# Kernel optimization log

Measured on AMD Instinct MI355X. Metric: run time of the kernel, lower is better.

Reference implementation:

```python
import jax, jax.numpy as jnp
import numpy as np

L = 16      # number of prior layers backsubstituted through (layer_idx)
D = 1024    # uniform layer width


def setup_inputs() -> dict:
    key = jax.random.key(0)
    ks = jax.random.split(key, 8)
    weights = jax.random.normal(ks[0], (D, D), jnp.float32) / np.sqrt(D)
    biases = jax.random.normal(ks[1], (D, 1), jnp.float32)
    net_x_lowers = jax.random.normal(ks[2], (L, D, D), jnp.float32) / np.sqrt(D)
    net_x_uppers = jax.random.normal(ks[3], (L, D, D), jnp.float32) / np.sqrt(D)
    net_b_lowers = jax.random.normal(ks[4], (L, D, 1), jnp.float32)
    net_b_uppers = jax.random.normal(ks[5], (L, D, 1), jnp.float32)
    input_lowers = jax.random.normal(ks[6], (D, 1), jnp.float32)
    input_uppers = input_lowers + jax.random.uniform(ks[7], (D, 1), jnp.float32)
    return {
        "weights": weights,
        "biases": biases,
        "net_x_lowers": net_x_lowers,
        "net_x_uppers": net_x_uppers,
        "net_b_lowers": net_b_lowers,
        "net_b_uppers": net_b_uppers,
        "input_lowers": input_lowers,
        "input_uppers": input_uppers,
    }


def _backsubstitute(weights, biases, net_x_lowers, net_x_uppers,
                    net_b_lowers, net_b_uppers, input_lowers, input_uppers):
    # Initial relational bounds of the affine layer: y = W^T x + b exactly.
    x0 = weights.T  # (out, in)

    def step(carry, layer):
        xl, xu, bl, bu = carry
        A_lo, A_up, c_lo, c_up = layer
        pl = jnp.maximum(xl, 0.0)
        nl = jnp.minimum(xl, 0.0)
        pu = jnp.maximum(xu, 0.0)
        nu = jnp.minimum(xu, 0.0)
        # intercept accumulation (signed split)
        bl = bl + pl @ c_lo + nl @ c_up
        bu = bu + pu @ c_up + nu @ c_lo
        # coefficient backsubstitution (signed split)
        xl = pl @ A_lo + nl @ A_up
        xu = pu @ A_up + nu @ A_lo
        return (xl, xu, bl, bu), None

    # Loop order: network[layer_idx - i] for i = 0..L-1; the stacked arrays are
    # ordered so index i corresponds to layer (layer_idx - i).
    (xl, xu, bl, bu), _ = jax.lax.scan(
        step,
        (x0, x0, biases, biases),
        (net_x_lowers, net_x_uppers, net_b_lowers, net_b_uppers),
    )

    lo_T = input_lowers.T  # (1, d0)
    up_T = input_uppers.T
    lowers = jnp.sum(jnp.maximum(xl, 0.0) * lo_T + jnp.minimum(xl, 0.0) * up_T,
                     axis=1, keepdims=True) + bl
    uppers = jnp.sum(jnp.maximum(xu, 0.0) * up_T + jnp.minimum(xu, 0.0) * lo_T,
                     axis=1, keepdims=True) + bu
    return jnp.stack([lowers, uppers])  # (2, D, 1)


def reference(weights, biases, net_x_lowers, net_x_uppers,
              net_b_lowers, net_b_uppers, input_lowers, input_uppers):
    return _backsubstitute(weights, biases, net_x_lowers, net_x_uppers,
                           net_b_lowers, net_b_uppers, input_lowers, input_uppers)
```

## Files before the change

### kernel.cpp

```cpp
#include <hip/hip_runtime.h>


#define DD 1024
#define LL 16

typedef _Float16 f16x8 __attribute__((ext_vector_type(8)));
typedef _Float16 f16x4 __attribute__((ext_vector_type(4)));
typedef float f32x4 __attribute__((ext_vector_type(4)));

__device__ __forceinline__ void gload16(const void* gsrc, void* ldst) {
  __builtin_amdgcn_global_load_lds(
      (const __attribute__((address_space(1))) unsigned int*)gsrc,
      (__attribute__((address_space(3))) unsigned int*)ldst, 16, 0, 0);
}

struct GemmTabs {
  const _Float16* xs[2][6];
  const _Float16* as[2][6];
};

template<int NSPLIT>
__global__ __launch_bounds__(256)
void gemm_step(GemmTabs tabs, float* __restrict__ part)
{
  constexpr int KSPL = 6144 / NSPLIT;
  constexpr int NIT  = KSPL / 32;
  constexpr int NZ   = 2 * NSPLIT;

  __shared__ _Float16 smX[2][8][512];
  __shared__ _Float16 smA[2][8][512];

  const int tid  = threadIdx.x;
  const int w    = tid >> 6;
  const int lane = tid & 63;
  const int ln15 = lane & 15;
  const int lhi  = lane >> 4;

  const int lin = blockIdx.x + gridDim.x * (blockIdx.y + gridDim.y * blockIdx.z);
  const int zz  = lin % NZ;
  const int ij  = lin / NZ;
  const int j0  = (ij & 7) * 128;
  const int i0  = (ij >> 3) * 128;
  const int lu    = zz >> (NSPLIT == 6 ? 0 : 0) ? 0 : 0;
  const int lu_   = zz / NSPLIT;
  const int split = zz % NSPLIT;

  const _Float16* const* xtab = tabs.xs[lu_];
  const _Float16* const* atab = tabs.as[lu_];

  const int wm = w >> 1, wn = w & 1;

  const int kbase = split * KSPL;
  const int seg0  = kbase >> 10;
  const int segB_ = (seg0 + 1 < 6) ? seg0 + 1 : 5;
  const int it_sw = (((seg0 + 1) << 10) - kbase) >> 5;
  const _Float16* xpA = xtab[seg0];
  const _Float16* apA = atab[seg0];
  const _Float16* xpB = xtab[segB_];
  const _Float16* apB = atab[segB_];

  f32x4 acc[4][4];
#pragma unroll
  for (int a = 0; a < 4; ++a)
#pragma unroll
    for (int b = 0; b < 4; ++b) acc[a][b] = (f32x4){0.f, 0.f, 0.f, 0.f};

  const int b_it = (4096 - kbase) >> 5;

  auto stage = [&](int buf, int it) {
    const _Float16* xp = (it < it_sw) ? xpA : xpB;
    const _Float16* ap = (it < it_sw) ? apA : apB;
    const int kcol = ((kbase + it * 32) & 1023) + lhi * 8;
#pragma unroll
    for (int r = 0; r < 4; ++r) {
      const int f = r * 4 + w;
      if (f < 8)
        gload16(xp + (size_t)(i0 + f * 16 + ln15) * DD + kcol, &smX[buf][f & 7][0]);
      else
        gload16(ap + (size_t)(j0 + (f - 8) * 16 + ln15) * DD + kcol, &smA[buf][f & 7][0]);
    }
  };

  stage(0, 0);

  int buf = 0;
  for (int it = 0; it < NIT; ++it) {
    if (it + 1 < NIT) {
      stage(buf ^ 1, it + 1);
      asm volatile("s_waitcnt vmcnt(4)" ::: "memory");
    } else {
      asm volatile("s_waitcnt vmcnt(0)" ::: "memory");
    }
    __builtin_amdgcn_s_barrier();
    __builtin_amdgcn_sched_barrier(0);

    if (it == b_it) {
#pragma unroll
      for (int a = 0; a < 4; ++a)
#pragma unroll
        for (int b = 0; b < 4; ++b) acc[a][b] *= (1.f / 2048.f);
    }

    f16x8 xf[4], af[4];
#pragma unroll
    for (int mi = 0; mi < 4; ++mi)
      xf[mi] = *(const f16x8*)&smX[buf][wm * 4 + mi][lane * 8];
#pragma unroll
    for (int ni = 0; ni < 4; ++ni)
      af[ni] = *(const f16x8*)&smA[buf][wn * 4 + ni][lane * 8];
#pragma unroll
    for (int mi = 0; mi < 4; ++mi)
#pragma unroll
      for (int ni = 0; ni < 4; ++ni)
        acc[mi][ni] = __builtin_amdgcn_mfma_f32_16x16x32_f16(xf[mi], af[ni], acc[mi][ni], 0, 0, 0);

    __builtin_amdgcn_sched_barrier(0);
    if (it + 1 < NIT) __builtin_amdgcn_s_barrier();
    buf ^= 1;
  }

  const float eps = (b_it >= NIT) ? (1.f / 2048.f) : 1.f;
  float* outp = part + ((size_t)(split * 2 + lu_) << 20);
#pragma unroll
  for (int mi = 0; mi < 4; ++mi) {
    const int r0 = i0 + wm * 64 + mi * 16 + lhi * 4;
#pragma unroll
    for (int ni = 0; ni < 4; ++ni) {
      const int c = j0 + wn * 64 + ni * 16 + ln15;
#pragma unroll
      for (int e = 0; e < 4; ++e)
        outp[(size_t)(r0 + e) * DD + c] = acc[mi][ni][e] * eps;
    }
  }
}

template<int NS>
__global__ __launch_bounds__(256)
void convert_prep(int direct,
                  const float* __restrict__ xt, const float* __restrict__ part,
                  const float* __restrict__ cl, const float* __restrict__ cu,
                  _Float16* __restrict__ pl1, _Float16* __restrict__ pl2,
                  _Float16* __restrict__ nl1, _Float16* __restrict__ nl2,
                  _Float16* __restrict__ pu1, _Float16* __restrict__ pu2,
                  _Float16* __restrict__ nu1, _Float16* __restrict__ nu2,
                  float* __restrict__ bl, float* __restrict__ bu,
                  const float* __restrict__ AloN, const float* __restrict__ AupN,
                  _Float16* __restrict__ L1, _Float16* __restrict__ L2,
                  _Float16* __restrict__ U1, _Float16* __restrict__ U2)
{
  __shared__ float shmem[64][68];
  const int t = threadIdx.x;

  if (blockIdx.x < 1024) {
    const int i = blockIdx.x;
    const int k = t * 4;
    const size_t off = (size_t)i * DD + k;

    float Yl[4], Yu[4];
    if (direct) {
      const float4 y = *(const float4*)&xt[off];
      Yl[0] = Yu[0] = y.x; Yl[1] = Yu[1] = y.y; Yl[2] = Yu[2] = y.z; Yl[3] = Yu[3] = y.w;
    } else {
#pragma unroll
      for (int e = 0; e < 4; ++e) { Yl[e] = 0.f; Yu[e] = 0.f; }
#pragma unroll
      for (int s = 0; s < NS; ++s) {
        const float4 a = *(const float4*)&part[((size_t)(s * 2 + 0) << 20) + off];
        const float4 b = *(const float4*)&part[((size_t)(s * 2 + 1) << 20) + off];
        Yl[0] += a.x; Yl[1] += a.y; Yl[2] += a.z; Yl[3] += a.w;
        Yu[0] += b.x; Yu[1] += b.y; Yu[2] += b.z; Yu[3] += b.w;
      }
    }

    const float4 c4l = *(const float4*)&cl[k];
    const float4 c4u = *(const float4*)&cu[k];
    const float Cl[4] = {c4l.x, c4l.y, c4l.z, c4l.w};
    const float Cu[4] = {c4u.x, c4u.y, c4u.z, c4u.w};

    f16x4 o_pl1, o_pl2, o_nl1, o_nl2, o_pu1, o_pu2, o_nu1, o_nu2;
    float blp = 0.f, bup = 0.f;
#pragma unroll
    for (int e = 0; e < 4; ++e) {
      const float pl = fmaxf(Yl[e], 0.f), nl = fminf(Yl[e], 0.f);
      const float pu = fmaxf(Yu[e], 0.f), nu = fminf(Yu[e], 0.f);
      blp += pl * Cl[e] + nl * Cu[e];
      bup += pu * Cu[e] + nu * Cl[e];
      _Float16 h;
      h = (_Float16)pl; o_pl1[e] = h; o_pl2[e] = (_Float16)((pl - (float)h) * 2048.f);
      h = (_Float16)nl; o_nl1[e] = h; o_nl2[e] = (_Float16)((nl - (float)h) * 2048.f);
      h = (_Float16)pu; o_pu1[e] = h; o_pu2[e] = (_Float16)((pu - (float)h) * 2048.f);
      h = (_Float16)nu; o_nu1[e] = h; o_nu2[e] = (_Float16)((nu - (float)h) * 2048.f);
    }
    *(f16x4*)&pl1[off] = o_pl1;  *(f16x4*)&pl2[off] = o_pl2;
    *(f16x4*)&nl1[off] = o_nl1;  *(f16x4*)&nl2[off] = o_nl2;
    *(f16x4*)&pu1[off] = o_pu1;  *(f16x4*)&pu2[off] = o_pu2;
    *(f16x4*)&nu1[off] = o_nu1;  *(f16x4*)&nu2[off] = o_nu2;

#pragma unroll
    for (int o = 32; o > 0; o >>= 1) {
      blp += __shfl_down(blp, o, 64);
      bup += __shfl_down(bup, o, 64);
    }
    if ((t & 63) == 0) { shmem[0][t >> 6] = blp; shmem[1][t >> 6] = bup; }
    __syncthreads();
    if (t == 0) {
      bl[i] += shmem[0][0] + shmem[0][1] + shmem[0][2] + shmem[0][3];
      bu[i] += shmem[1][0] + shmem[1][1] + shmem[1][2] + shmem[1][3];
    }
  } else {
    const int r = blockIdx.x - 1024;
    const int k0 = (r & 15) * 64;
    const int n0 = ((r >> 4) & 15) * 64;
    const int zz = r >> 8;
    const int rid = t >> 4, cid = t & 15;
    const float* src = zz ? AupN : AloN;
    _Float16* d1 = zz ? U1 : L1;
    _Float16* d2 = zz ? U2 : L2;
#pragma unroll
    for (int rr = 0; rr < 4; ++rr) {
      const int kk = rid * 4 + rr;
      *(float4*)&shmem[kk][cid * 4] = *(const float4*)&src[(size_t)(k0 + kk) * DD + n0 + cid * 4];
    }
    __syncthreads();
#pragma unroll
    for (int rr = 0; rr < 4; ++rr) {
      const int n = rid * 4 + rr;
      f16x4 v1, v2;
#pragma unroll
      for (int e = 0; e < 4; ++e) {
        const float v = shmem[cid * 4 + e][n];
        const _Float16 h = (_Float16)v;
        v1[e] = h;
        v2[e] = (_Float16)((v - (float)h) * 2048.f);
      }
      const size_t o = (size_t)(n0 + n) * DD + k0 + cid * 4;
      *(f16x4*)&d1[o] = v1;
      *(f16x4*)&d2[o] = v2;
    }
  }
}

__global__ __launch_bounds__(256)
void transpose_w(const float* __restrict__ W, float* __restrict__ xt)
{
  __shared__ float tile[32][33];
  const int x  = blockIdx.x * 32 + threadIdx.x;
  const int y0 = blockIdx.y * 32 + threadIdx.y;
#pragma unroll
  for (int r = 0; r < 32; r += 8)
    tile[threadIdx.y + r][threadIdx.x] = W[(size_t)(y0 + r) * DD + x];
  __syncthreads();
  const int xo  = blockIdx.y * 32 + threadIdx.x;
  const int yo0 = blockIdx.x * 32 + threadIdx.y;
#pragma unroll
  for (int r = 0; r < 32; r += 8)
    xt[(size_t)(yo0 + r) * DD + xo] = tile[threadIdx.x][threadIdx.y + r];
}

template<int NS>
__global__ __launch_bounds__(256)
void bs_final2(const float* __restrict__ part,
               const float* __restrict__ bl, const float* __restrict__ bu,
               const float* __restrict__ inLo, const float* __restrict__ inUp,
               float* __restrict__ out)
{
  const int i = blockIdx.x;
  const int t = threadIdx.x;
  const int k = t * 4;
  const size_t off = (size_t)i * DD + k;
  float Xl[4] = {0.f, 0.f, 0.f, 0.f}, Xu[4] = {0.f, 0.f, 0.f, 0.f};
#pragma unroll
  for (int s = 0; s < NS; ++s) {
    const float4 a = *(const float4*)&part[((size_t)(s * 2 + 0) << 20) + off];
    const float4 b = *(const float4*)&part[((size_t)(s * 2 + 1) << 20) + off];
    Xl[0] += a.x; Xl[1] += a.y; Xl[2] += a.z; Xl[3] += a.w;
    Xu[0] += b.x; Xu[1] += b.y; Xu[2] += b.z; Xu[3] += b.w;
  }
  const float4 lo4 = *(const float4*)&inLo[k];
  const float4 up4 = *(const float4*)&inUp[k];
  const float Lo[4] = {lo4.x, lo4.y, lo4.z, lo4.w};
  const float Up[4] = {up4.x, up4.y, up4.z, up4.w};
  float sl = 0.f, su = 0.f;
#pragma unroll
  for (int e = 0; e < 4; ++e) {
    sl += fmaxf(Xl[e], 0.f) * Lo[e] + fminf(Xl[e], 0.f) * Up[e];
    su += fmaxf(Xu[e], 0.f) * Up[e] + fminf(Xu[e], 0.f) * Lo[e];
  }
#pragma unroll
  for (int o = 32; o > 0; o >>= 1) {
    sl += __shfl_down(sl, o, 64);
    su += __shfl_down(su, o, 64);
  }
  __shared__ float red[2][4];
  if ((t & 63) == 0) { red[0][t >> 6] = sl; red[1][t >> 6] = su; }
  __syncthreads();
  if (t == 0) {
    out[i]      = red[0][0] + red[0][1] + red[0][2] + red[0][3] + bl[i];
    out[DD + i] = red[1][0] + red[1][1] + red[1][2] + red[1][3] + bu[i];
  }
}

#define BM 64
#define BN 64
#define BK 16
#define TM 4
#define TN 4
#define XPAD 4
#define XSTRIDE (BM + XPAD)

struct alignas(16) StepSmem {
  float xl[2][BK][XSTRIDE];
  float xu[2][BK][XSTRIDE];
  float alo[2][BK][BN];
  float aup[2][BK][BN];
  float clo[2][BK];
  float cup[2][BK];
  float bred[8][64];
};

__global__ __launch_bounds__(256)
void bs_step(const float* __restrict__ Xl, const float* __restrict__ Xu,
             float* __restrict__ Yl, float* __restrict__ Yu,
             const float* __restrict__ Alo, const float* __restrict__ Aup,
             const float* __restrict__ Clo, const float* __restrict__ Cup,
             float* __restrict__ bl, float* __restrict__ bu)
{
  __shared__ StepSmem sm;
  const int tid = threadIdx.x;
  const int tx = tid & 15;
  const int ty = tid >> 4;
  const int i0 = blockIdx.y * BM;
  const int j0 = blockIdx.x * BN;
  const bool doBias = (blockIdx.x == 0);
  const int xrow = tid >> 2;
  const int xseg = tid & 3;
  const int arow = tid >> 4;
  const int acol = (tid & 15) * 4;
  const int brow = tid & 63;
  const int bq   = tid >> 6;

  float accl[TM][TN] = {};
  float accu[TM][TN] = {};
  float blp = 0.f, bup = 0.f;
  float4 rxl, rxu, ral, rau;
  float  rc = 0.f;

  auto load_panel = [&](int kp) {
    rxl = *(const float4*)&Xl[(size_t)(i0 + xrow) * DD + kp + xseg * 4];
    rxu = *(const float4*)&Xu[(size_t)(i0 + xrow) * DD + kp + xseg * 4];
    ral = *(const float4*)&Alo[(size_t)(kp + arow) * DD + j0 + acol];
    rau = *(const float4*)&Aup[(size_t)(kp + arow) * DD + j0 + acol];
    if (tid < 32) rc = (tid < 16) ? Clo[kp + tid] : Cup[kp + tid - 16];
  };
  auto store_panel = [&](int b) {
    const float* pxl = (const float*)&rxl;
    const float* pxu = (const float*)&rxu;
#pragma unroll
    for (int s2 = 0; s2 < 4; ++s2) {
      sm.xl[b][xseg * 4 + s2][xrow] = pxl[s2];
      sm.xu[b][xseg * 4 + s2][xrow] = pxu[s2];
    }
    *(float4*)&sm.alo[b][arow][acol] = ral;
    *(float4*)&sm.aup[b][arow][acol] = rau;
    if (tid < 16)      sm.clo[b][tid] = rc;
    else if (tid < 32) sm.cup[b][tid - 16] = rc;
  };

  load_panel(0);
  store_panel(0);
  __syncthreads();

  constexpr int NP = DD / BK;
  for (int p = 0; p < NP; ++p) {
    const int buf = p & 1;
    const bool more = (p + 1 < NP);
    if (more) load_panel((p + 1) * BK);
#pragma unroll 4
    for (int k = 0; k < BK; ++k) {
      const float4 xl4 = *(const float4*)&sm.xl[buf][k][ty * TM];
      const float4 xu4 = *(const float4*)&sm.xu[buf][k][ty * TM];
      const float4 al4 = *(const float4*)&sm.alo[buf][k][tx * TN];
      const float4 au4 = *(const float4*)&sm.aup[buf][k][tx * TN];
      const float xlv[TM] = {xl4.x, xl4.y, xl4.z, xl4.w};
      const float xuv[TM] = {xu4.x, xu4.y, xu4.z, xu4.w};
      const float alv[TN] = {al4.x, al4.y, al4.z, al4.w};
      const float auv[TN] = {au4.x, au4.y, au4.z, au4.w};
#pragma unroll
      for (int m = 0; m < TM; ++m) {
        const float pl = fmaxf(xlv[m], 0.f), nl = fminf(xlv[m], 0.f);
        const float pu = fmaxf(xuv[m], 0.f), nu = fminf(xuv[m], 0.f);
#pragma unroll
        for (int n = 0; n < TN; ++n) {
          accl[m][n] = fmaf(pl, alv[n], fmaf(nl, auv[n], accl[m][n]));
          accu[m][n] = fmaf(pu, auv[n], fmaf(nu, alv[n], accu[m][n]));
        }
      }
    }
    if (doBias) {
#pragma unroll
      for (int kk = 0; kk < 4; ++kk) {
        const int k = bq * 4 + kk;
        const float xlv = sm.xl[buf][k][brow];
        const float xuv = sm.xu[buf][k][brow];
        const float cl = sm.clo[buf][k], cu = sm.cup[buf][k];
        blp += fmaxf(xlv, 0.f) * cl + fminf(xlv, 0.f) * cu;
        bup += fmaxf(xuv, 0.f) * cu + fminf(xuv, 0.f) * cl;
      }
    }
    if (more) store_panel(buf ^ 1);
    __syncthreads();
  }

#pragma unroll
  for (int m = 0; m < TM; ++m) {
    *(float4*)&Yl[(size_t)(i0 + ty * TM + m) * DD + j0 + tx * TN] =
        make_float4(accl[m][0], accl[m][1], accl[m][2], accl[m][3]);
    *(float4*)&Yu[(size_t)(i0 + ty * TM + m) * DD + j0 + tx * TN] =
        make_float4(accu[m][0], accu[m][1], accu[m][2], accu[m][3]);
  }
  if (doBias) {
    sm.bred[bq][brow]     = blp;
    sm.bred[4 + bq][brow] = bup;
    __syncthreads();
    if (tid < 64) {
      const int i = i0 + tid;
      bl[i] += sm.bred[0][tid] + sm.bred[1][tid] + sm.bred[2][tid] + sm.bred[3][tid];
      bu[i] += sm.bred[4][tid] + sm.bred[5][tid] + sm.bred[6][tid] + sm.bred[7][tid];
    }
  }
}

__global__ __launch_bounds__(256)
void bs_transpose_init(const float* __restrict__ W,
                       float* __restrict__ xl, float* __restrict__ xu)
{
  __shared__ float tile[32][33];
  const int x  = blockIdx.x * 32 + threadIdx.x;
  const int y0 = blockIdx.y * 32 + threadIdx.y;
#pragma unroll
  for (int r = 0; r < 32; r += 8)
    tile[threadIdx.y + r][threadIdx.x] = W[(size_t)(y0 + r) * DD + x];
  __syncthreads();
  const int xo  = blockIdx.y * 32 + threadIdx.x;
  const int yo0 = blockIdx.x * 32 + threadIdx.y;
#pragma unroll
  for (int r = 0; r < 32; r += 8) {
    const float v = tile[threadIdx.x][threadIdx.y + r];
    xl[(size_t)(yo0 + r) * DD + xo] = v;
    xu[(size_t)(yo0 + r) * DD + xo] = v;
  }
}

__global__ __launch_bounds__(256)
void bs_final(const float* __restrict__ Xl, const float* __restrict__ Xu,
              const float* __restrict__ bl, const float* __restrict__ bu,
              const float* __restrict__ inLo, const float* __restrict__ inUp,
              float* __restrict__ out)
{
  __shared__ float red[2][4];
  const int i = blockIdx.x;
  const int tid = threadIdx.x;
  const float4 xl4 = *(const float4*)&Xl[(size_t)i * DD + tid * 4];
  const float4 xu4 = *(const float4*)&Xu[(size_t)i * DD + tid * 4];
  const float4 lo4 = *(const float4*)&inLo[tid * 4];
  const float4 up4 = *(const float4*)&inUp[tid * 4];
  const float xlv[4] = {xl4.x, xl4.y, xl4.z, xl4.w};
  const float xuv[4] = {xu4.x, xu4.y, xu4.z, xu4.w};
  const float lov[4] = {lo4.x, lo4.y, lo4.z, lo4.w};
  const float upv[4] = {up4.x, up4.y, up4.z, up4.w};
  float sl = 0.f, su = 0.f;
#pragma unroll
  for (int c = 0; c < 4; ++c) {
    sl += fmaxf(xlv[c], 0.f) * lov[c] + fminf(xlv[c], 0.f) * upv[c];
    su += fmaxf(xuv[c], 0.f) * upv[c] + fminf(xuv[c], 0.f) * lov[c];
  }
#pragma unroll
  for (int off = 32; off > 0; off >>= 1) {
    sl += __shfl_down(sl, off, 64);
    su += __shfl_down(su, off, 64);
  }
  if ((tid & 63) == 0) { red[0][tid >> 6] = sl; red[1][tid >> 6] = su; }
  __syncthreads();
  if (tid == 0) {
    out[i]      = red[0][0] + red[0][1] + red[0][2] + red[0][3] + bl[i];
    out[DD + i] = red[1][0] + red[1][1] + red[1][2] + red[1][3] + bu[i];
  }
}

template<int NS>
static void run_f16(const float* W, const float* biases,
                    const float* AloAll, const float* AupAll,
                    const float* CloAll, const float* CupAll,
                    const float* inLo, const float* inUp,
                    float* out, char* ws, hipStream_t stream)
{
  float*     part = (float*)ws;
  _Float16*  xpl  = (_Float16*)(ws + ((size_t)NS * 8ull << 20));
  _Float16*  apl  = (_Float16*)(ws + (((size_t)NS * 8ull + 16) << 20));
  float*     bl   = (float*)(ws + (((size_t)NS * 8ull + 24) << 20));
  float*     bu   = bl + DD;
  float*     XT   = part;

  auto P = [&](int idx) { return xpl + (size_t)idx * (1u << 20); };
  _Float16 *pl1 = P(0), *pl2 = P(1), *nl1 = P(2), *nl2 = P(3);
  _Float16 *pu1 = P(4), *pu2 = P(5), *nu1 = P(6), *nu2 = P(7);
  _Float16 *AL1 = apl, *AL2 = apl + (1u << 20), *AU1 = apl + (2u << 20), *AU2 = apl + (3u << 20);

  GemmTabs tabs;
  const _Float16* xs0[6] = {pl1, pl2, nl1, nl2, pl1, nl1};
  const _Float16* as0[6] = {AL2, AL1, AU2, AU1, AL1, AU1};
  const _Float16* xs1[6] = {pu1, pu2, nu1, nu2, pu1, nu1};
  const _Float16* as1[6] = {AU2, AU1, AL2, AL1, AU1, AL1};
  for (int s = 0; s < 6; ++s) {
    tabs.xs[0][s] = xs0[s]; tabs.as[0][s] = as0[s];
    tabs.xs[1][s] = xs1[s]; tabs.as[1][s] = as1[s];
  }

  transpose_w<<<dim3(32, 32), dim3(32, 8), 0, stream>>>(W, XT);
  hipMemcpyAsync(bl, biases, DD * sizeof(float), hipMemcpyDeviceToDevice, stream);
  hipMemcpyAsync(bu, biases, DD * sizeof(float), hipMemcpyDeviceToDevice, stream);

  convert_prep<NS><<<1536, 256, 0, stream>>>(1, XT, part, CloAll, CupAll,
                                             pl1, pl2, nl1, nl2, pu1, pu2, nu1, nu2, bl, bu,
                                             AloAll, AupAll, AL1, AL2, AU1, AU2);
  for (int s = 0; s < LL; ++s) {
    gemm_step<NS><<<dim3(8, 8, 2 * NS), 256, 0, stream>>>(tabs, part);
    if (s < LL - 1)
      convert_prep<NS><<<1536, 256, 0, stream>>>(0, XT, part,
                                                 CloAll + (size_t)(s + 1) * DD,
                                                 CupAll + (size_t)(s + 1) * DD,
                                                 pl1, pl2, nl1, nl2, pu1, pu2, nu1, nu2, bl, bu,
                                                 AloAll + (size_t)(s + 1) * DD * DD,
                                                 AupAll + (size_t)(s + 1) * DD * DD,
                                                 AL1, AL2, AU1, AU2);
  }
  bs_final2<NS><<<DD, 256, 0, stream>>>(part, bl, bu, inLo, inUp, out);
}

extern "C" void kernel_launch(void* const* d_in, const int* in_sizes, int n_in,
                              void* d_out, int out_size, void* d_ws, size_t ws_size,
                              hipStream_t stream)
{
  const float* W      = (const float*)d_in[0];
  const float* biases = (const float*)d_in[1];
  const float* AloAll = (const float*)d_in[2];
  const float* AupAll = (const float*)d_in[3];
  const float* CloAll = (const float*)d_in[4];
  const float* CupAll = (const float*)d_in[5];
  const float* inLo   = (const float*)d_in[6];
  const float* inUp   = (const float*)d_in[7];
  float* out = (float*)d_out;

  const size_t NEED6 = (72ull << 20) + 8192;
  const size_t NEED4 = (56ull << 20) + 8192;

  if (ws_size >= NEED6) {
    run_f16<6>(W, biases, AloAll, AupAll, CloAll, CupAll, inLo, inUp, out, (char*)d_ws, stream);
    return;
  }
  if (ws_size >= NEED4) {
    run_f16<4>(W, biases, AloAll, AupAll, CloAll, CupAll, inLo, inUp, out, (char*)d_ws, stream);
    return;
  }

  float* ws  = (float*)d_ws;
  float* XA  = ws;
  float* XuA = ws + (size_t)DD * DD;
  float* XB  = ws + 2ull * DD * DD;
  float* XuB = ws + 3ull * DD * DD;
  float* bl  = ws + 4ull * DD * DD;
  float* bu  = bl + DD;
  bs_transpose_init<<<dim3(DD / 32, DD / 32), dim3(32, 8), 0, stream>>>(W, XA, XuA);
  hipMemcpyAsync(bl, biases, DD * sizeof(float), hipMemcpyDeviceToDevice, stream);
  hipMemcpyAsync(bu, biases, DD * sizeof(float), hipMemcpyDeviceToDevice, stream);
  const float* xi  = XA;  const float* xui = XuA;
  float*       xo  = XB;  float*       xuo = XuB;
  for (int l = 0; l < LL; ++l) {
    bs_step<<<dim3(DD / BN, DD / BM), 256, 0, stream>>>(
        xi, xui, xo, xuo,
        AloAll + (size_t)l * DD * DD, AupAll + (size_t)l * DD * DD,
        CloAll + (size_t)l * DD,      CupAll + (size_t)l * DD, bl, bu);
    const float* txi = xi; const float* txui = xui;
    xi = xo; xui = xuo;
    xo = (float*)txi; xuo = (float*)txui;
  }
  bs_final<<<DD, 256, 0, stream>>>(xi, xui, bl, bu, inLo, inUp, out);
}
```

Baseline: 1.210 ms.

## Add 256x128-tile triple-buffered GEMM kernel with 512 threads and fixed 4-way split-K

Adds a new GEMM kernel that uses 256x128 output tiles, 512 threads, a 64-wide K step and three LDS buffers in dynamic shared memory. It prefetches two stages ahead with explicit vmcnt waits and raises wave priority during the MFMA block. The host always uses a 4-way K split, and a fallback kernel covers the case where the shared-memory attribute cannot be set. The goal is more data reuse per tile and deeper load/compute overlap. In exchange the grid shrinks to 256 blocks and each block needs more LDS, which limits occupancy.

```diff
diff --git a/kernel.cpp b/kernel.cpp
--- a/kernel.cpp
+++ b/kernel.cpp
@@ -19,29 +19,155 @@
   const _Float16* as[2][6];
 };
 
-template<int NSPLIT>
-__global__ __launch_bounds__(256)
-void gemm_step(GemmTabs tabs, float* __restrict__ part)
-{
-  constexpr int KSPL = 6144 / NSPLIT;
-  constexpr int NIT  = KSPL / 32;
-  constexpr int NZ   = 2 * NSPLIT;
-
-  __shared__ _Float16 smX[2][8][512];
-  __shared__ _Float16 smA[2][8][512];
+struct SM8 {
+  _Float16 x[3][32][512];
+  _Float16 a[3][16][512];
+};
+
+__global__ __launch_bounds__(512, 2)
+void gemm_step8(GemmTabs tabs, float* __restrict__ part)
+{
+  extern __shared__ char dynsm[];
+  SM8& sm = *reinterpret_cast<SM8*>(dynsm);
 
   const int tid  = threadIdx.x;
   const int w    = tid >> 6;
   const int lane = tid & 63;
   const int ln15 = lane & 15;
   const int lhi  = lane >> 4;
+  const int wm   = w >> 1;
+  const int wn   = w & 1;
+
+  const int lin = blockIdx.x;
+  const int zz  = lin & 7;
+  const int ij  = lin >> 3;
+  const int i0  = (ij >> 3) * 256;
+  const int j0  = (ij & 7) * 128;
+  const int lu    = zz >> 2;
+  const int split = zz & 3;
+
+  constexpr int NT = 24;
+  const int kbase = split * 1536;
+  const int seg0  = kbase >> 10;
+  const int seg1  = (seg0 + 1 < 6) ? seg0 + 1 : 5;
+  const int it_sw = (((seg0 + 1) << 10) - kbase) >> 6;
+  const _Float16* xpA = tabs.xs[lu][seg0];
+  const _Float16* apA = tabs.as[lu][seg0];
+  const _Float16* xpB = tabs.xs[lu][seg1];
+  const _Float16* apB = tabs.as[lu][seg1];
+  const int b_it = (4096 - kbase) >> 6;
+
+  f32x4 acc[4][4];
+#pragma unroll
+  for (int a = 0; a < 4; ++a)
+#pragma unroll
+    for (int b = 0; b < 4; ++b) acc[a][b] = (f32x4){0.f, 0.f, 0.f, 0.f};
+
+  auto stage6 = [&](int slot, int t) {
+    const _Float16* xp = (t < it_sw) ? xpA : xpB;
+    const _Float16* ap = (t < it_sw) ? apA : apB;
+    const int kcol = ((kbase + t * 64) & 1023) + lhi * 8;
+#pragma unroll
+    for (int r = 0; r < 6; ++r) {
+      const int g = r * 8 + w;
+      if (g < 32) {
+        gload16(xp + (size_t)(i0 + (g >> 1) * 16 + ln15) * DD + kcol + (g & 1) * 32,
+                &sm.x[slot][g][0]);
+      } else {
+        const int gg = g - 32;
+        gload16(ap + (size_t)(j0 + (gg >> 1) * 16 + ln15) * DD + kcol + (gg & 1) * 32,
+                &sm.a[slot][gg][0]);
+      }
+    }
+  };
+
+  stage6(0, 0);
+  stage6(1, 1);
+
+  int cur = 0;
+#pragma unroll 1
+  for (int t = 0; t < NT; ++t) {
+    if (t + 2 < NT) {
+      int s2 = cur + 2; if (s2 >= 3) s2 -= 3;
+      stage6(s2, t + 2);
+      asm volatile("s_waitcnt vmcnt(12)" ::: "memory");
+    } else if (t + 2 == NT) {
+      asm volatile("s_waitcnt vmcnt(6)" ::: "memory");
+    } else {
+      asm volatile("s_waitcnt vmcnt(0)" ::: "memory");
+    }
+    __builtin_amdgcn_s_barrier();
+    __builtin_amdgcn_sched_barrier(0);
+
+    if (t == b_it) {
+#pragma unroll
+      for (int a = 0; a < 4; ++a)
+#pragma unroll
+        for (int b = 0; b < 4; ++b) acc[a][b] *= (1.f / 2048.f);
+    }
+
+    f16x8 xf[2][4], af[2][4];
+#pragma unroll
+    for (int kc = 0; kc < 2; ++kc) {
+#pragma unroll
+      for (int mi = 0; mi < 4; ++mi)
+        xf[kc][mi] = *(const f16x8*)&sm.x[cur][(wm * 4 + mi) * 2 + kc][lane * 8];
+#pragma unroll
+      for (int ni = 0; ni < 4; ++ni)
+        af[kc][ni] = *(const f16x8*)&sm.a[cur][(wn * 4 + ni) * 2 + kc][lane * 8];
+    }
+    __builtin_amdgcn_s_setprio(1);
+#pragma unroll
+    for (int kc = 0; kc < 2; ++kc)
+#pragma unroll
+      for (int mi = 0; mi < 4; ++mi)
+#pragma unroll
+        for (int ni = 0; ni < 4; ++ni)
+          acc[mi][ni] = __builtin_amdgcn_mfma_f32_16x16x32_f16(xf[kc][mi], af[kc][ni], acc[mi][ni], 0, 0, 0);
+    __builtin_amdgcn_s_setprio(0);
+
+    __builtin_amdgcn_sched_barrier(0);
+    __builtin_amdgcn_s_barrier();
+    cur = (cur == 2) ? 0 : cur + 1;
+  }
+
+  const float eps = (b_it >= NT) ? (1.f / 2048.f) : 1.f;
+  float* outp = part + ((size_t)(split * 2 + lu) << 20);
+#pragma unroll
+  for (int mi = 0; mi < 4; ++mi) {
+    const int r0 = i0 + wm * 64 + mi * 16 + lhi * 4;
+#pragma unroll
+    for (int ni = 0; ni < 4; ++ni) {
+      const int c = j0 + wn * 64 + ni * 16 + ln15;
+#pragma unroll
+      for (int e = 0; e < 4; ++e)
+        outp[(size_t)(r0 + e) * DD + c] = acc[mi][ni][e] * eps;
+    }
+  }
+}
+
+template<int NSPLIT>
+__global__ __launch_bounds__(256)
+void gemm_step(GemmTabs tabs, float* __restrict__ part)
+{
+  constexpr int KSPL = 6144 / NSPLIT;
+  constexpr int NIT  = KSPL / 32;
+  constexpr int NZ   = 2 * NSPLIT;
+
+  __shared__ _Float16 smX[2][8][512];
+  __shared__ _Float16 smA[2][8][512];
+
+  const int tid  = threadIdx.x;
+  const int w    = tid >> 6;
+  const int lane = tid & 63;
+  const int ln15 = lane & 15;
+  const int lhi  = lane >> 4;
 
   const int lin = blockIdx.x + gridDim.x * (blockIdx.y + gridDim.y * blockIdx.z);
   const int zz  = lin % NZ;
   const int ij  = lin / NZ;
   const int j0  = (ij & 7) * 128;
   const int i0  = (ij >> 3) * 128;
-  const int lu    = zz >> (NSPLIT == 6 ? 0 : 0) ? 0 : 0;
   const int lu_   = zz / NSPLIT;
   const int split = zz % NSPLIT;
 
@@ -487,56 +613,6 @@
   }
 }
 
-template<int NS>
-static void run_f16(const float* W, const float* biases,
-                    const float* AloAll, const float* AupAll,
-                    const float* CloAll, const float* CupAll,
-                    const float* inLo, const float* inUp,
-                    float* out, char* ws, hipStream_t stream)
-{
-  float*     part = (float*)ws;
-  _Float16*  xpl  = (_Float16*)(ws + ((size_t)NS * 8ull << 20));
-  _Float16*  apl  = (_Float16*)(ws + (((size_t)NS * 8ull + 16) << 20));
-  float*     bl   = (float*)(ws + (((size_t)NS * 8ull + 24) << 20));
-  float*     bu   = bl + DD;
-  float*     XT   = part;
-
-  auto P = [&](int idx) { return xpl + (size_t)idx * (1u << 20); };
-  _Float16 *pl1 = P(0), *pl2 = P(1), *nl1 = P(2), *nl2 = P(3);
-  _Float16 *pu1 = P(4), *pu2 = P(5), *nu1 = P(6), *nu2 = P(7);
-  _Float16 *AL1 = apl, *AL2 = apl + (1u << 20), *AU1 = apl + (2u << 20), *AU2 = apl + (3u << 20);
-
-  GemmTabs tabs;
-  const _Float16* xs0[6] = {pl1, pl2, nl1, nl2, pl1, nl1};
-  const _Float16* as0[6] = {AL2, AL1, AU2, AU1, AL1, AU1};
-  const _Float16* xs1[6] = {pu1, pu2, nu1, nu2, pu1, nu1};
-  const _Float16* as1[6] = {AU2, AU1, AL2, AL1, AU1, AL1};
-  for (int s = 0; s < 6; ++s) {
-    tabs.xs[0][s] = xs0[s]; tabs.as[0][s] = as0[s];
-    tabs.xs[1][s] = xs1[s]; tabs.as[1][s] = as1[s];
-  }
-
-  transpose_w<<<dim3(32, 32), dim3(32, 8), 0, stream>>>(W, XT);
-  hipMemcpyAsync(bl, biases, DD * sizeof(float), hipMemcpyDeviceToDevice, stream);
-  hipMemcpyAsync(bu, biases, DD * sizeof(float), hipMemcpyDeviceToDevice, stream);
-
-  convert_prep<NS><<<1536, 256, 0, stream>>>(1, XT, part, CloAll, CupAll,
-                                             pl1, pl2, nl1, nl2, pu1, pu2, nu1, nu2, bl, bu,
-                                             AloAll, AupAll, AL1, AL2, AU1, AU2);
-  for (int s = 0; s < LL; ++s) {
-    gemm_step<NS><<<dim3(8, 8, 2 * NS), 256, 0, stream>>>(tabs, part);
-    if (s < LL - 1)
-      convert_prep<NS><<<1536, 256, 0, stream>>>(0, XT, part,
-                                                 CloAll + (size_t)(s + 1) * DD,
-                                                 CupAll + (size_t)(s + 1) * DD,
-                                                 pl1, pl2, nl1, nl2, pu1, pu2, nu1, nu2, bl, bu,
-                                                 AloAll + (size_t)(s + 1) * DD * DD,
-                                                 AupAll + (size_t)(s + 1) * DD * DD,
-                                                 AL1, AL2, AU1, AU2);
-  }
-  bs_final2<NS><<<DD, 256, 0, stream>>>(part, bl, bu, inLo, inUp, out);
-}
-
 extern "C" void kernel_launch(void* const* d_in, const int* in_sizes, int n_in,
                               void* d_out, int out_size, void* d_ws, size_t ws_size,
                               hipStream_t stream)
@@ -551,38 +627,80 @@
   const float* inUp   = (const float*)d_in[7];
   float* out = (float*)d_out;
 
-  const size_t NEED6 = (72ull << 20) + 8192;
-  const size_t NEED4 = (56ull << 20) + 8192;
-
-  if (ws_size >= NEED6) {
-    run_f16<6>(W, biases, AloAll, AupAll, CloAll, CupAll, inLo, inUp, out, (char*)d_ws, stream);
+  const size_t NEED = (56ull << 20) + 8192;
+  if (ws_size < NEED) {
+    float* wsf = (float*)d_ws;
+    float* XA  = wsf;
+    float* XuA = wsf + (size_t)DD * DD;
+    float* XB  = wsf + 2ull * DD * DD;
+    float* XuB = wsf + 3ull * DD * DD;
+    float* bl  = wsf + 4ull * DD * DD;
+    float* bu  = bl + DD;
+    bs_transpose_init<<<dim3(DD / 32, DD / 32), dim3(32, 8), 0, stream>>>(W, XA, XuA);
+    hipMemcpyAsync(bl, biases, DD * sizeof(float), hipMemcpyDeviceToDevice, stream);
+    hipMemcpyAsync(bu, biases, DD * sizeof(float), hipMemcpyDeviceToDevice, stream);
+    const float* xi  = XA;  const float* xui = XuA;
+    float*       xo  = XB;  float*       xuo = XuB;
+    for (int l = 0; l < LL; ++l) {
+      bs_step<<<dim3(DD / BN, DD / BM), 256, 0, stream>>>(
+          xi, xui, xo, xuo,
+          AloAll + (size_t)l * DD * DD, AupAll + (size_t)l * DD * DD,
+          CloAll + (size_t)l * DD,      CupAll + (size_t)l * DD, bl, bu);
+      const float* txi = xi; const float* txui = xui;
+      xi = xo; xui = xuo;
+      xo = (float*)txi; xuo = (float*)txui;
+    }
+    bs_final<<<DD, 256, 0, stream>>>(xi, xui, bl, bu, inLo, inUp, out);
     return;
   }
-  if (ws_size >= NEED4) {
-    run_f16<4>(W, biases, AloAll, AupAll, CloAll, CupAll, inLo, inUp, out, (char*)d_ws, stream);
-    return;
-  }
-
-  float* ws  = (float*)d_ws;
-  float* XA  = ws;
-  float* XuA = ws + (size_t)DD * DD;
-  float* XB  = ws + 2ull * DD * DD;
-  float* XuB = ws + 3ull * DD * DD;
-  float* bl  = ws + 4ull * DD * DD;
-  float* bu  = bl + DD;
-  bs_transpose_init<<<dim3(DD / 32, DD / 32), dim3(32, 8), 0, stream>>>(W, XA, XuA);
+
+  char* ws = (char*)d_ws;
+  float*     part = (float*)ws;
+  _Float16*  xpl  = (_Float16*)(ws + (32ull << 20));
+  _Float16*  apl  = (_Float16*)(ws + (48ull << 20));
+  float*     bl   = (float*)(ws + (56ull << 20));
+  float*     bu   = bl + DD;
+  float*     XT   = part;
+
+  auto P = [&](int idx) { return xpl + (size_t)idx * (1u << 20); };
+  _Float16 *pl1 = P(0), *pl2 = P(1), *nl1 = P(2), *nl2 = P(3);
+  _Float16 *pu1 = P(4), *pu2 = P(5), *nu1 = P(6), *nu2 = P(7);
+  _Float16 *AL1 = apl, *AL2 = apl + (1u << 20), *AU1 = apl + (2u << 20), *AU2 = apl + (3u << 20);
+
+  GemmTabs tabs;
+  const _Float16* xs0[6] = {pl1, pl2, nl1, nl2, pl1, nl1};
+  const _Float16* as0[6] = {AL2, AL1, AU2, AU1, AL1, AU1};
+  const _Float16* xs1[6] = {pu1, pu2, nu1, nu2, pu1, nu1};
+  const _Float16* as1[6] = {AU2, AU1, AL2, AL1, AU1, AL1};
+  for (int s = 0; s < 6; ++s) {
+    tabs.xs[0][s] = xs0[s]; tabs.as[0][s] = as0[s];
+    tabs.xs[1][s] = xs1[s]; tabs.as[1][s] = as1[s];
+  }
+
+  const hipError_t attr_ok = hipFuncSetAttribute(
+      reinterpret_cast<const void*>(&gemm_step8),
+      hipFuncAttributeMaxDynamicSharedMemorySize, (int)sizeof(SM8));
+
+  transpose_w<<<dim3(32, 32), dim3(32, 8), 0, stream>>>(W, XT);
   hipMemcpyAsync(bl, biases, DD * sizeof(float), hipMemcpyDeviceToDevice, stream);
   hipMemcpyAsync(bu, biases, DD * sizeof(float), hipMemcpyDeviceToDevice, stream);
-  const float* xi  = XA;  const float* xui = XuA;
-  float*       xo  = XB;  float*       xuo = XuB;
-  for (int l = 0; l < LL; ++l) {
-    bs_step<<<dim3(DD / BN, DD / BM), 256, 0, stream>>>(
-        xi, xui, xo, xuo,
-        AloAll + (size_t)l * DD * DD, AupAll + (size_t)l * DD * DD,
-        CloAll + (size_t)l * DD,      CupAll + (size_t)l * DD, bl, bu);
-    const float* txi = xi; const float* txui = xui;
-    xi = xo; xui = xuo;
-    xo = (float*)txi; xuo = (float*)txui;
-  }
-  bs_final<<<DD, 256, 0, stream>>>(xi, xui, bl, bu, inLo, inUp, out);
-}
+
+  convert_prep<4><<<1536, 256, 0, stream>>>(1, XT, part, CloAll, CupAll,
+                                            pl1, pl2, nl1, nl2, pu1, pu2, nu1, nu2, bl, bu,
+                                            AloAll, AupAll, AL1, AL2, AU1, AU2);
+  for (int s = 0; s < LL; ++s) {
+    if (attr_ok == hipSuccess)
+      gemm_step8<<<256, 512, sizeof(SM8), stream>>>(tabs, part);
+    else
+      gemm_step<4><<<dim3(8, 8, 8), 256, 0, stream>>>(tabs, part);
+    if (s < LL - 1)
+      convert_prep<4><<<1536, 256, 0, stream>>>(0, XT, part,
+                                                CloAll + (size_t)(s + 1) * DD,
+                                                CupAll + (size_t)(s + 1) * DD,
+                                                pl1, pl2, nl1, nl2, pu1, pu2, nu1, nu2, bl, bu,
+                                                AloAll + (size_t)(s + 1) * DD * DD,
+                                                AupAll + (size_t)(s + 1) * DD * DD,
+                                                AL1, AL2, AU1, AU2);
+  }
+  bs_final2<4><<<DD, 256, 0, stream>>>(part, bl, bu, inLo, inUp, out);
+}
```

Measured after the change: 993.1 us. 1.22x faster.

## Replace LDS-staged split-K GEMM with register-direct MFMA kernel for six-way split

Applied to the files above, without the earlier changes.

Adds a GEMM kernel that loads f16 fragments directly from global memory into registers with double buffering, skipping LDS staging and barriers, and uses it when the six-way split path is selected. Each block handles one full K segment, so segment-switching logic is removed and a per-segment scale factor is applied at store. This trades LDS-based reuse for relying on cache to serve repeated fragment loads, and requests higher occupancy via launch bounds.

```diff
diff --git a/kernel.cpp b/kernel.cpp
--- a/kernel.cpp
+++ b/kernel.cpp
@@ -7,41 +7,122 @@
 typedef _Float16 f16x8 __attribute__((ext_vector_type(8)));
 typedef _Float16 f16x4 __attribute__((ext_vector_type(4)));
 typedef float f32x4 __attribute__((ext_vector_type(4)));
-
-__device__ __forceinline__ void gload16(const void* gsrc, void* ldst) {
-  __builtin_amdgcn_global_load_lds(
-      (const __attribute__((address_space(1))) unsigned int*)gsrc,
-      (__attribute__((address_space(3))) unsigned int*)ldst, 16, 0, 0);
-}
 
 struct GemmTabs {
   const _Float16* xs[2][6];
   const _Float16* as[2][6];
 };
 
-template<int NSPLIT>
-__global__ __launch_bounds__(256)
-void gemm_step(GemmTabs tabs, float* __restrict__ part)
-{
-  constexpr int KSPL = 6144 / NSPLIT;
-  constexpr int NIT  = KSPL / 32;
-  constexpr int NZ   = 2 * NSPLIT;
-
-  __shared__ _Float16 smX[2][8][512];
-  __shared__ _Float16 smA[2][8][512];
-
+__global__ __launch_bounds__(256, 3)
+void gemm_reg(GemmTabs tabs, float* __restrict__ part)
+{
   const int tid  = threadIdx.x;
   const int w    = tid >> 6;
   const int lane = tid & 63;
   const int ln15 = lane & 15;
   const int lhi  = lane >> 4;
+  const int wm   = w >> 1, wn = w & 1;
+
+  const int lin = blockIdx.x;
+  const int zz  = lin % 12;
+  const int ij  = lin / 12;
+  const int j0  = (ij & 7) * 128;
+  const int i0  = (ij >> 3) * 128;
+  const int lu    = zz / 6;
+  const int split = zz % 6;
+
+  const _Float16* xp = tabs.xs[lu][split];
+  const _Float16* ap = tabs.as[lu][split];
+  const float eps = (split < 4) ? (1.f / 2048.f) : 1.f;
+
+  const _Float16* xb[4];
+  const _Float16* ab[4];
+#pragma unroll
+  for (int mi = 0; mi < 4; ++mi)
+    xb[mi] = xp + (size_t)(i0 + wm * 64 + mi * 16 + ln15) * DD + lhi * 8;
+#pragma unroll
+  for (int ni = 0; ni < 4; ++ni)
+    ab[ni] = ap + (size_t)(j0 + wn * 64 + ni * 16 + ln15) * DD + lhi * 8;
+
+  f32x4 acc[4][4];
+#pragma unroll
+  for (int a = 0; a < 4; ++a)
+#pragma unroll
+    for (int b = 0; b < 4; ++b) acc[a][b] = (f32x4){0.f, 0.f, 0.f, 0.f};
+
+  f16x8 fxA[4], faA[4], fxB[4], faB[4];
+
+#pragma unroll
+  for (int mi = 0; mi < 4; ++mi) fxA[mi] = *(const f16x8*)(xb[mi]);
+#pragma unroll
+  for (int ni = 0; ni < 4; ++ni) faA[ni] = *(const f16x8*)(ab[ni]);
+
+#pragma unroll 1
+  for (int it = 0; it < 32; it += 2) {
+#pragma unroll
+    for (int mi = 0; mi < 4; ++mi) fxB[mi] = *(const f16x8*)(xb[mi] + (it + 1) * 32);
+#pragma unroll
+    for (int ni = 0; ni < 4; ++ni) faB[ni] = *(const f16x8*)(ab[ni] + (it + 1) * 32);
+#pragma unroll
+    for (int mi = 0; mi < 4; ++mi)
+#pragma unroll
+      for (int ni = 0; ni < 4; ++ni)
+        acc[mi][ni] = __builtin_amdgcn_mfma_f32_16x16x32_f16(fxA[mi], faA[ni], acc[mi][ni], 0, 0, 0);
+
+    const int itn = (it + 2 < 32) ? it + 2 : 30;
+#pragma unroll
+    for (int mi = 0; mi < 4; ++mi) fxA[mi] = *(const f16x8*)(xb[mi] + itn * 32);
+#pragma unroll
+    for (int ni = 0; ni < 4; ++ni) faA[ni] = *(const f16x8*)(ab[ni] + itn * 32);
+#pragma unroll
+    for (int mi = 0; mi < 4; ++mi)
+#pragma unroll
+      for (int ni = 0; ni < 4; ++ni)
+        acc[mi][ni] = __builtin_amdgcn_mfma_f32_16x16x32_f16(fxB[mi], faB[ni], acc[mi][ni], 0, 0, 0);
+  }
+
+  float* outp = part + ((size_t)(split * 2 + lu) << 20);
+#pragma unroll
+  for (int mi = 0; mi < 4; ++mi) {
+    const int r0 = i0 + wm * 64 + mi * 16 + lhi * 4;
+#pragma unroll
+    for (int ni = 0; ni < 4; ++ni) {
+      const int c = j0 + wn * 64 + ni * 16 + ln15;
+#pragma unroll
+      for (int e = 0; e < 4; ++e)
+        outp[(size_t)(r0 + e) * DD + c] = acc[mi][ni][e] * eps;
+    }
+  }
+}
+
+__device__ __forceinline__ void gload16(const void* gsrc, void* ldst) {
+  __builtin_amdgcn_global_load_lds(
+      (const __attribute__((address_space(1))) unsigned int*)gsrc,
+      (__attribute__((address_space(3))) unsigned int*)ldst, 16, 0, 0);
+}
+
+template<int NSPLIT>
+__global__ __launch_bounds__(256)
+void gemm_step(GemmTabs tabs, float* __restrict__ part)
+{
+  constexpr int KSPL = 6144 / NSPLIT;
+  constexpr int NIT  = KSPL / 32;
+  constexpr int NZ   = 2 * NSPLIT;
+
+  __shared__ _Float16 smX[2][8][512];
+  __shared__ _Float16 smA[2][8][512];
+
+  const int tid  = threadIdx.x;
+  const int w    = tid >> 6;
+  const int lane = tid & 63;
+  const int ln15 = lane & 15;
+  const int lhi  = lane >> 4;
 
   const int lin = blockIdx.x + gridDim.x * (blockIdx.y + gridDim.y * blockIdx.z);
   const int zz  = lin % NZ;
   const int ij  = lin / NZ;
   const int j0  = (ij & 7) * 128;
   const int i0  = (ij >> 3) * 128;
-  const int lu    = zz >> (NSPLIT == 6 ? 0 : 0) ? 0 : 0;
   const int lu_   = zz / NSPLIT;
   const int split = zz % NSPLIT;
 
@@ -524,7 +605,10 @@
                                              pl1, pl2, nl1, nl2, pu1, pu2, nu1, nu2, bl, bu,
                                              AloAll, AupAll, AL1, AL2, AU1, AU2);
   for (int s = 0; s < LL; ++s) {
-    gemm_step<NS><<<dim3(8, 8, 2 * NS), 256, 0, stream>>>(tabs, part);
+    if (NS == 6)
+      gemm_reg<<<768, 256, 0, stream>>>(tabs, part);
+    else
+      gemm_step<NS><<<dim3(8, 8, 2 * NS), 256, 0, stream>>>(tabs, part);
     if (s < LL - 1)
       convert_prep<NS><<<1536, 256, 0, stream>>>(0, XT, part,
                                                  CloAll + (size_t)(s + 1) * DD,
@@ -563,12 +647,12 @@
     return;
   }
 
-  float* ws  = (float*)d_ws;
-  float* XA  = ws;
-  float* XuA = ws + (size_t)DD * DD;
-  float* XB  = ws + 2ull * DD * DD;
-  float* XuB = ws + 3ull * DD * DD;
-  float* bl  = ws + 4ull * DD * DD;
+  float* wsf = (float*)d_ws;
+  float* XA  = wsf;
+  float* XuA = wsf + (size_t)DD * DD;
+  float* XB  = wsf + 2ull * DD * DD;
+  float* XuB = wsf + 3ull * DD * DD;
+  float* bl  = wsf + 4ull * DD * DD;
   float* bu  = bl + DD;
   bs_transpose_init<<<dim3(DD / 32, DD / 32), dim3(32, 8), 0, stream>>>(W, XA, XuA);
   hipMemcpyAsync(bl, biases, DD * sizeof(float), hipMemcpyDeviceToDevice, stream);
```

Result: slower. 1.875 ms (+55.0%).
